# Performance work log

Hardware: AMD Instinct MI355X
Metric: run time of the kernel (lower is better)

Reference implementation:

```python
import jax, jax.numpy as jnp
import numpy as np

B, L, H = 2, 2048, 2048
NH, KVH = 16, 4
D = H // NH          # 128
G = NH // KVH        # 4 query heads per kv head
LN_EPS = 1e-12


def setup_inputs() -> dict:
    key = jax.random.key(0)
    ks = jax.random.split(key, 6)
    s = 0.02
    return {
        "hidden_state": jax.random.normal(ks[0], (B, L, H), jnp.float32),
        "mask": jnp.zeros((B, 1, 1, L), jnp.float32),
        "Wq": jax.random.normal(ks[1], (H, H), jnp.float32) * s,
        "bq": jnp.zeros((H,), jnp.float32),
        "Wk": jax.random.normal(ks[2], (KVH * D, H), jnp.float32) * s,
        "bk": jnp.zeros((KVH * D,), jnp.float32),
        "Wv": jax.random.normal(ks[3], (KVH * D, H), jnp.float32) * s,
        "bv": jnp.zeros((KVH * D,), jnp.float32),
        "Wo": jax.random.normal(ks[4], (H, H), jnp.float32) * s,
        "bo": jnp.zeros((H,), jnp.float32),
        "ln_g": jnp.ones((H,), jnp.float32),
        "ln_b": jnp.zeros((H,), jnp.float32),
    }


def _layernorm(x, g, b):
    mu = jnp.mean(x, axis=-1, keepdims=True)
    var = jnp.mean(jnp.square(x - mu), axis=-1, keepdims=True)
    return (x - mu) * jax.lax.rsqrt(var + LN_EPS) * g + b


def reference(hidden_state, mask, Wq, bq, Wk, bk, Wv, bv, Wo, bo, ln_g, ln_b):
    x = hidden_state
    # projections: b l (h d)
    q = x @ Wq.T + bq            # [B,L,NH*D]
    k = x @ Wk.T + bk            # [B,L,KVH*D]
    v = x @ Wv.T + bv            # [B,L,KVH*D]
    # b l (h d) -> b h l d, with q heads grouped per kv head (GQA broadcast,
    # mathematically identical to repeat_kv + dense SDPA)
    q = q.reshape(B, L, KVH, G, D).transpose(0, 2, 3, 1, 4)   # [B,KVH,G,L,D]
    k = k.reshape(B, L, KVH, D).transpose(0, 2, 1, 3)         # [B,KVH,L,D]
    v = v.reshape(B, L, KVH, D).transpose(0, 2, 1, 3)         # [B,KVH,L,D]
    scale = 1.0 / jnp.sqrt(jnp.float32(D))
    scores = jnp.einsum('bkgld,bkmd->bkglm', q, k) * scale    # [B,KVH,G,L,L]
    scores = scores + mask[:, :, None]                         # broadcast [B,1,1,1,L]
    attn = jax.nn.softmax(scores, axis=-1)
    out = jnp.einsum('bkglm,bkmd->bkgld', attn, v)            # [B,KVH,G,L,D]
    out = out.transpose(0, 3, 1, 2, 4).reshape(B, L, H)       # b h l d -> b l (h d)
    # SelfOutput: dense + residual + layernorm
    out = out @ Wo.T + bo
    return _layernorm(out + x, ln_g, ln_b)
```

## Files before the change

kernel.cpp:

```cpp
#include <hip/hip_runtime.h>
#include <math.h>

typedef short v8s __attribute__((ext_vector_type(8)));
typedef float v4f __attribute__((ext_vector_type(4)));
typedef unsigned long long ull;

constexpr int L_ = 2048;
constexpr int H_ = 2048;
constexpr float LOG2E = 1.4426950408889634f;
constexpr float QSCALE = 0.08838834764831845f * LOG2E;

__device__ inline unsigned short f2bf(float f) {
    unsigned int u = __float_as_uint(f);
    u += 0x7fffu + ((u >> 16) & 1u);
    return (unsigned short)(u >> 16);
}

__device__ inline void async16(const void* g, void* l) {
    __builtin_amdgcn_global_load_lds(
        (const __attribute__((address_space(1))) unsigned int*)g,
        (__attribute__((address_space(3))) unsigned int*)l, 16, 0, 0);
}

__global__ __launch_bounds__(256) void conv_f32_bf16(
    const float* __restrict__ src, unsigned short* __restrict__ dst, int n8)
{
    int i = blockIdx.x * 256 + threadIdx.x;
    if (i >= n8) return;
    float4 a = *(const float4*)(src + (size_t)i * 8);
    float4 b = *(const float4*)(src + (size_t)i * 8 + 4);
    v8s o;
    o[0] = (short)f2bf(a.x); o[1] = (short)f2bf(a.y);
    o[2] = (short)f2bf(a.z); o[3] = (short)f2bf(a.w);
    o[4] = (short)f2bf(b.x); o[5] = (short)f2bf(b.y);
    o[6] = (short)f2bf(b.z); o[7] = (short)f2bf(b.w);
    *(v8s*)(dst + (size_t)i * 8) = o;
}

template <int MODE>
__global__ __launch_bounds__(256) void gemm_mfma(
    const unsigned short* __restrict__ A, const unsigned short* __restrict__ W,
    const float* __restrict__ b0, const float* __restrict__ b1,
    const float* __restrict__ b2,
    unsigned short* __restrict__ oq, unsigned short* __restrict__ ok,
    unsigned short* __restrict__ ovt,
    float* __restrict__ of, const float* __restrict__ resid,
    int K, int N)
{
    __shared__ short A_s[128 * 32];
    __shared__ short B_s[128 * 32];

    const int tid  = threadIdx.x;
    const int lane = tid & 63;
    const int wave = tid >> 6;
    const int lid  = lane & 15;
    const int g    = lane >> 4;
    const int wr   = wave >> 1, wc = wave & 1;
    const int row0 = blockIdx.y * 128, col0 = blockIdx.x * 128;

    v4f acc[4][4];
#pragma unroll
    for (int i = 0; i < 4; ++i)
#pragma unroll
        for (int j = 0; j < 4; ++j) acc[i][j] = (v4f){0.f, 0.f, 0.f, 0.f};

    for (int k0 = 0; k0 < K; k0 += 32) {
        __syncthreads();
#pragma unroll
        for (int i = 0; i < 2; ++i) {
            int idx = tid + i * 256;
            int r = idx >> 2, s = idx & 3;
            int c = s ^ ((r >> 1) & 3);
            async16(A + (size_t)(row0 + r) * K + k0 + c * 8, &A_s[idx * 8]);
            async16(W + (size_t)(col0 + r) * K + k0 + c * 8, &B_s[idx * 8]);
        }
        __syncthreads();

        v8s af[4], bf[4];
#pragma unroll
        for (int t = 0; t < 4; ++t) {
            int ra = wr * 64 + t * 16 + lid;
            int rb = wc * 64 + t * 16 + lid;
            af[t] = *(const v8s*)&A_s[ra * 32 + ((g ^ ((ra >> 1) & 3)) * 8)];
            bf[t] = *(const v8s*)&B_s[rb * 32 + ((g ^ ((rb >> 1) & 3)) * 8)];
        }
#pragma unroll
        for (int mt = 0; mt < 4; ++mt)
#pragma unroll
            for (int nt = 0; nt < 4; ++nt)
                acc[mt][nt] = __builtin_amdgcn_mfma_f32_16x16x32_bf16(
                    af[mt], bf[nt], acc[mt][nt], 0, 0, 0);
    }

    const int crow = row0 + wr * 64, ccol = col0 + wc * 64;
    if (MODE == 0) {
#pragma unroll
        for (int mt = 0; mt < 4; ++mt)
#pragma unroll
            for (int nt = 0; nt < 4; ++nt) {
                int cc = ccol + nt * 16 + lid;
                float bb = b0[cc];
#pragma unroll
                for (int r = 0; r < 4; ++r) {
                    int rr = crow + mt * 16 + g * 4 + r;
                    of[(size_t)rr * N + cc] =
                        acc[mt][nt][r] + bb + resid[(size_t)rr * N + cc];
                }
            }
    } else {
        const int seg = (col0 < 2048) ? 0 : (col0 < 2560 ? 1 : 2);
#pragma unroll
        for (int mt = 0; mt < 4; ++mt)
#pragma unroll
            for (int nt = 0; nt < 4; ++nt) {
                int cc = ccol + nt * 16 + lid;
                if (seg == 0) {
                    float bb = b0[cc];
#pragma unroll
                    for (int r = 0; r < 4; ++r) {
                        int rr = crow + mt * 16 + g * 4 + r;
                        oq[(size_t)rr * 2048 + cc] =
                            f2bf((acc[mt][nt][r] + bb) * QSCALE);
                    }
                } else if (seg == 1) {
                    float bb = b1[cc - 2048];
#pragma unroll
                    for (int r = 0; r < 4; ++r) {
                        int rr = crow + mt * 16 + g * 4 + r;
                        ok[(size_t)rr * 512 + (cc - 2048)] =
                            f2bf(acc[mt][nt][r] + bb);
                    }
                } else {
                    float bb = b2[cc - 2560];
#pragma unroll
                    for (int r = 0; r < 4; ++r) {
                        int rr = crow + mt * 16 + g * 4 + r;
                        ovt[((size_t)((rr >> 11) * 512 + (cc - 2560))) * 2048 +
                            (rr & 2047)] = f2bf(acc[mt][nt][r] + bb);
                    }
                }
            }
    }
}

__global__ __launch_bounds__(256) void flash_mfma(
    const unsigned short* __restrict__ Q,
    const unsigned short* __restrict__ K,
    const unsigned short* __restrict__ Vt,
    const float* __restrict__ mask,
    unsigned short* __restrict__ AO)
{
    __shared__ short K_s[64 * 128];
    __shared__ short V_s[128 * 64];
    __shared__ short P_s[128 * 64];
    __shared__ float mask_s[64];
    __shared__ float alpha_s[128];
    __shared__ float l_s[128];

    const int tid  = threadIdx.x;
    const int lane = tid & 63;
    const int wave = tid >> 6;
    const int lid  = lane & 15;
    const int g    = lane >> 4;
    const int h    = blockIdx.y;
    const int b    = blockIdx.z;
    const int kvh  = h >> 2;
    const int q0   = blockIdx.x * 128;
    const int wq   = wave * 32;

    v8s bq[2][4];
    {
        const size_t base = ((size_t)(b * L_ + q0 + wq + lid)) * 2048 + h * 128;
#pragma unroll
        for (int qt = 0; qt < 2; ++qt)
#pragma unroll
            for (int kc = 0; kc < 4; ++kc)
                bq[qt][kc] = *(const v8s*)(Q + base + (size_t)qt * 16 * 2048 +
                                           kc * 32 + g * 8);
    }

    v4f oacc[2][8];
#pragma unroll
    for (int mt = 0; mt < 2; ++mt)
#pragma unroll
        for (int nt = 0; nt < 8; ++nt) oacc[mt][nt] = (v4f){0.f, 0.f, 0.f, 0.f};
    float m2[2] = {-1e30f, -1e30f};
    float lsm[2] = {0.f, 0.f};

    for (int k0 = 0; k0 < L_; k0 += 64) {
        __syncthreads();
#pragma unroll
        for (int i = 0; i < 4; ++i) {
            int idx = tid + i * 256;
            int kr = idx >> 4, ks = idx & 15;
            int kc = ks ^ (kr & 15);
            async16(K + ((size_t)(b * L_ + k0 + kr)) * 512 + kvh * 128 + kc * 8,
                    &K_s[idx * 8]);
            int vd = idx >> 3, vs = idx & 7;
            int vc = vs ^ (vd & 7);
            async16(Vt + ((size_t)(b * 512 + kvh * 128 + vd)) * 2048 + k0 + vc * 8,
                    &V_s[idx * 8]);
        }
        if (tid < 16) {
            float4 mv = *(const float4*)(mask + (size_t)b * L_ + k0 + tid * 4);
            mask_s[tid * 4 + 0] = mv.x * LOG2E;
            mask_s[tid * 4 + 1] = mv.y * LOG2E;
            mask_s[tid * 4 + 2] = mv.z * LOG2E;
            mask_s[tid * 4 + 3] = mv.w * LOG2E;
        }
        __syncthreads();

        v4f sacc[4][2];
#pragma unroll
        for (int kt = 0; kt < 4; ++kt)
#pragma unroll
            for (int qt = 0; qt < 2; ++qt) sacc[kt][qt] = (v4f){0.f, 0.f, 0.f, 0.f};
#pragma unroll
        for (int kc = 0; kc < 4; ++kc) {
#pragma unroll
            for (int kt = 0; kt < 4; ++kt) {
                v8s ak = *(const v8s*)&K_s[(kt * 16 + lid) * 128 +
                                           (((kc * 4 + g) ^ lid) * 8)];
#pragma unroll
                for (int qt = 0; qt < 2; ++qt)
                    sacc[kt][qt] = __builtin_amdgcn_mfma_f32_16x16x32_bf16(
                        ak, bq[qt][kc], sacc[kt][qt], 0, 0, 0);
            }
        }

        float pmax[2] = {-1e30f, -1e30f};
#pragma unroll
        for (int kt = 0; kt < 4; ++kt) {
            float4 mk = *(const float4*)&mask_s[kt * 16 + g * 4];
#pragma unroll
            for (int qt = 0; qt < 2; ++qt) {
                sacc[kt][qt][0] += mk.x;
                sacc[kt][qt][1] += mk.y;
                sacc[kt][qt][2] += mk.z;
                sacc[kt][qt][3] += mk.w;
#pragma unroll
                for (int r = 0; r < 4; ++r)
                    pmax[qt] = fmaxf(pmax[qt], sacc[kt][qt][r]);
            }
        }
#pragma unroll
        for (int qt = 0; qt < 2; ++qt) {
            pmax[qt] = fmaxf(pmax[qt], __shfl_xor(pmax[qt], 16));
            pmax[qt] = fmaxf(pmax[qt], __shfl_xor(pmax[qt], 32));
        }
        float alpha[2], lad[2];
#pragma unroll
        for (int qt = 0; qt < 2; ++qt) {
            float mnew = fmaxf(m2[qt], pmax[qt]);
            alpha[qt] = __builtin_amdgcn_exp2f(m2[qt] - mnew);
            m2[qt] = mnew;
            lad[qt] = 0.f;
        }
#pragma unroll
        for (int kt = 0; kt < 4; ++kt)
#pragma unroll
            for (int qt = 0; qt < 2; ++qt)
#pragma unroll
                for (int r = 0; r < 4; ++r) {
                    float e = __builtin_amdgcn_exp2f(sacc[kt][qt][r] - m2[qt]);
                    sacc[kt][qt][r] = e;
                    lad[qt] += e;
                }
#pragma unroll
        for (int qt = 0; qt < 2; ++qt) {
            lad[qt] += __shfl_xor(lad[qt], 16);
            lad[qt] += __shfl_xor(lad[qt], 32);
            lsm[qt] = lsm[qt] * alpha[qt] + lad[qt];
        }

#pragma unroll
        for (int qt = 0; qt < 2; ++qt) {
            int qrow = wq + qt * 16 + lid;
#pragma unroll
            for (int kt = 0; kt < 4; ++kt) {
                ull pk = (ull)f2bf(sacc[kt][qt][0]) |
                         ((ull)f2bf(sacc[kt][qt][1]) << 16) |
                         ((ull)f2bf(sacc[kt][qt][2]) << 32) |
                         ((ull)f2bf(sacc[kt][qt][3]) << 48);
                int chunk = kt * 2 + (g >> 1);
                *(ull*)&P_s[qrow * 64 + ((chunk ^ (lid & 7)) * 8) + (g & 1) * 4] = pk;
            }
        }
        if (lane < 16) {
            alpha_s[wq + lid] = alpha[0];
            alpha_s[wq + 16 + lid] = alpha[1];
        }
        __syncthreads();

#pragma unroll
        for (int mt = 0; mt < 2; ++mt) {
            float4 al = *(const float4*)&alpha_s[wq + mt * 16 + g * 4];
            float a4[4] = {al.x, al.y, al.z, al.w};
#pragma unroll
            for (int nt = 0; nt < 8; ++nt)
#pragma unroll
                for (int r = 0; r < 4; ++r) oacc[mt][nt][r] *= a4[r];
        }
#pragma unroll
        for (int kc2 = 0; kc2 < 2; ++kc2) {
            int slot = ((kc2 * 4 + g) ^ (lid & 7)) * 8;
            v8s ap[2];
#pragma unroll
            for (int mt = 0; mt < 2; ++mt)
                ap[mt] = *(const v8s*)&P_s[(wq + mt * 16 + lid) * 64 + slot];
#pragma unroll
            for (int nt = 0; nt < 8; ++nt) {
                v8s bv = *(const v8s*)&V_s[(nt * 16 + lid) * 64 + slot];
#pragma unroll
                for (int mt = 0; mt < 2; ++mt)
                    oacc[mt][nt] = __builtin_amdgcn_mfma_f32_16x16x32_bf16(
                        ap[mt], bv, oacc[mt][nt], 0, 0, 0);
            }
        }
    }

    if (lane < 16) {
        l_s[wq + lid] = lsm[0];
        l_s[wq + 16 + lid] = lsm[1];
    }
    __syncthreads();
#pragma unroll
    for (int mt = 0; mt < 2; ++mt) {
        float4 lv = *(const float4*)&l_s[wq + mt * 16 + g * 4];
        float linv[4] = {1.f / lv.x, 1.f / lv.y, 1.f / lv.z, 1.f / lv.w};
#pragma unroll
        for (int nt = 0; nt < 8; ++nt)
#pragma unroll
            for (int r = 0; r < 4; ++r) {
                size_t orow = (size_t)(b * L_ + q0 + wq + mt * 16 + g * 4 + r);
                AO[orow * 2048 + h * 128 + nt * 16 + lid] =
                    f2bf(oacc[mt][nt][r] * linv[r]);
            }
    }
}

__global__ __launch_bounds__(256) void ln_kernel(
    const float* __restrict__ P, const float* __restrict__ g,
    const float* __restrict__ bta, float* __restrict__ Out)
{
    const int row = blockIdx.x;
    const int tid = threadIdx.x;
    const float* p = P + (size_t)row * H_;

    float vals[8];
    float s = 0.f;
#pragma unroll
    for (int it = 0; it < 2; ++it) {
        int c = tid * 4 + it * 1024;
        float4 a = *(const float4*)&p[c];
        vals[it * 4 + 0] = a.x; vals[it * 4 + 1] = a.y;
        vals[it * 4 + 2] = a.z; vals[it * 4 + 3] = a.w;
        s += a.x + a.y + a.z + a.w;
    }
    __shared__ float red[4];
    float t = s;
#pragma unroll
    for (int off = 32; off > 0; off >>= 1) t += __shfl_xor(t, off);
    if ((tid & 63) == 0) red[tid >> 6] = t;
    __syncthreads();
    float mean = (red[0] + red[1] + red[2] + red[3]) * (1.f / (float)H_);

    float vsum = 0.f;
#pragma unroll
    for (int i = 0; i < 8; ++i) {
        float d = vals[i] - mean;
        vsum += d * d;
    }
    __syncthreads();
    t = vsum;
#pragma unroll
    for (int off = 32; off > 0; off >>= 1) t += __shfl_xor(t, off);
    if ((tid & 63) == 0) red[tid >> 6] = t;
    __syncthreads();
    float var = (red[0] + red[1] + red[2] + red[3]) * (1.f / (float)H_);
    float rs  = 1.f / sqrtf(var + 1e-12f);

#pragma unroll
    for (int it = 0; it < 2; ++it) {
        int c = tid * 4 + it * 1024;
        float4 gv = *(const float4*)&g[c];
        float4 bv = *(const float4*)&bta[c];
        float4 ov;
        ov.x = (vals[it * 4 + 0] - mean) * rs * gv.x + bv.x;
        ov.y = (vals[it * 4 + 1] - mean) * rs * gv.y + bv.y;
        ov.z = (vals[it * 4 + 2] - mean) * rs * gv.z + bv.z;
        ov.w = (vals[it * 4 + 3] - mean) * rs * gv.w + bv.w;
        *(float4*)&Out[(size_t)row * H_ + c] = ov;
    }
}

extern "C" void kernel_launch(void* const* d_in, const int* in_sizes, int n_in,
                              void* d_out, int out_size, void* d_ws, size_t ws_size,
                              hipStream_t stream)
{
    const float* x    = (const float*)d_in[0];
    const float* mask = (const float*)d_in[1];
    const float* Wq   = (const float*)d_in[2];
    const float* bq   = (const float*)d_in[3];
    const float* Wk   = (const float*)d_in[4];
    const float* bk   = (const float*)d_in[5];
    const float* Wv   = (const float*)d_in[6];
    const float* bv   = (const float*)d_in[7];
    const float* Wo   = (const float*)d_in[8];
    const float* bo   = (const float*)d_in[9];
    const float* lng  = (const float*)d_in[10];
    const float* lnb  = (const float*)d_in[11];
    float* out = (float*)d_out;

    char* ws = (char*)d_ws;
    unsigned short* xb   = (unsigned short*)(ws);
    unsigned short* wqkv = (unsigned short*)(ws + 16777216);
    unsigned short* q    = (unsigned short*)(ws + 29360128);
    unsigned short* k    = (unsigned short*)(ws + 46137344);
    unsigned short* vt   = (unsigned short*)(ws + 50331648);
    unsigned short* ao   = (unsigned short*)(ws + 54525952);
    unsigned short* wob  = (unsigned short*)(ws + 71303168);
    float*          pj   = (float*)(ws);

    dim3 blk(256);
    conv_f32_bf16<<<4096, blk, 0, stream>>>(x,  xb,   1048576);
    conv_f32_bf16<<<2048, blk, 0, stream>>>(Wq, wqkv,            524288);
    conv_f32_bf16<<<512,  blk, 0, stream>>>(Wk, wqkv + 2048*2048, 131072);
    conv_f32_bf16<<<512,  blk, 0, stream>>>(Wv, wqkv + 2560*2048, 131072);
    conv_f32_bf16<<<2048, blk, 0, stream>>>(Wo, wob,             524288);

    gemm_mfma<3><<<dim3(24, 32), blk, 0, stream>>>(
        xb, wqkv, bq, bk, bv, q, k, vt, nullptr, nullptr, 2048, 3072);

    flash_mfma<<<dim3(16, 16, 2), blk, 0, stream>>>(q, k, vt, mask, ao);

    gemm_mfma<0><<<dim3(16, 32), blk, 0, stream>>>(
        ao, wob, bo, nullptr, nullptr, nullptr, nullptr, nullptr, pj, x, 2048, 2048);
    ln_kernel<<<4096, blk, 0, stream>>>(pj, lng, lnb, out);
}
```

Baseline: 427.6 us.

## Pipeline GEMM and flash loads, fuse conversions, add V transpose kernel

```diff
diff --git a/kernel.cpp b/kernel.cpp
--- a/kernel.cpp
+++ b/kernel.cpp
@@ -22,19 +22,39 @@
         (__attribute__((address_space(3))) unsigned int*)l, 16, 0, 0);
 }
 
-__global__ __launch_bounds__(256) void conv_f32_bf16(
-    const float* __restrict__ src, unsigned short* __restrict__ dst, int n8)
-{
-    int i = blockIdx.x * 256 + threadIdx.x;
-    if (i >= n8) return;
-    float4 a = *(const float4*)(src + (size_t)i * 8);
-    float4 b = *(const float4*)(src + (size_t)i * 8 + 4);
+__global__ __launch_bounds__(256) void conv_all(
+    const float* __restrict__ x,  const float* __restrict__ wq,
+    const float* __restrict__ wk, const float* __restrict__ wv,
+    const float* __restrict__ wo, const float* __restrict__ mask,
+    unsigned short* __restrict__ xb, unsigned short* __restrict__ wqkvb,
+    unsigned short* __restrict__ wob, float* __restrict__ maskL)
+{
+    int u = blockIdx.x * 256 + threadIdx.x;
+    const float* s;
+    unsigned short* d;
+    if (u < 1048576)      { s = x  + (size_t)u * 8;             d = xb   + (size_t)u * 8; }
+    else if (u < 1572864) { size_t t = (size_t)(u - 1048576) * 8; s = wq + t; d = wqkvb + t; }
+    else if (u < 1703936) { size_t t = (size_t)(u - 1572864) * 8; s = wk + t; d = wqkvb + (size_t)2048 * 2048 + t; }
+    else if (u < 1835008) { size_t t = (size_t)(u - 1703936) * 8; s = wv + t; d = wqkvb + (size_t)2560 * 2048 + t; }
+    else if (u < 2359296) { size_t t = (size_t)(u - 1835008) * 8; s = wo + t; d = wob + t; }
+    else if (u < 2359808) {
+        int m = (u - 2359296) * 8;
+        float4 a = *(const float4*)(mask + m);
+        float4 b = *(const float4*)(mask + m + 4);
+        float4 oa = {a.x * LOG2E, a.y * LOG2E, a.z * LOG2E, a.w * LOG2E};
+        float4 ob = {b.x * LOG2E, b.y * LOG2E, b.z * LOG2E, b.w * LOG2E};
+        *(float4*)(maskL + m) = oa;
+        *(float4*)(maskL + m + 4) = ob;
+        return;
+    } else return;
+    float4 a = *(const float4*)s;
+    float4 b = *(const float4*)(s + 4);
     v8s o;
     o[0] = (short)f2bf(a.x); o[1] = (short)f2bf(a.y);
     o[2] = (short)f2bf(a.z); o[3] = (short)f2bf(a.w);
     o[4] = (short)f2bf(b.x); o[5] = (short)f2bf(b.y);
     o[6] = (short)f2bf(b.z); o[7] = (short)f2bf(b.w);
-    *(v8s*)(dst + (size_t)i * 8) = o;
+    *(v8s*)d = o;
 }
 
 template <int MODE>
@@ -43,12 +63,11 @@
     const float* __restrict__ b0, const float* __restrict__ b1,
     const float* __restrict__ b2,
     unsigned short* __restrict__ oq, unsigned short* __restrict__ ok,
-    unsigned short* __restrict__ ovt,
+    unsigned short* __restrict__ ov,
     float* __restrict__ of, const float* __restrict__ resid,
     int K, int N)
 {
-    __shared__ short A_s[128 * 32];
-    __shared__ short B_s[128 * 32];
+    __shared__ short SM[3 * 8192];
 
     const int tid  = threadIdx.x;
     const int lane = tid & 63;
@@ -58,31 +77,44 @@
     const int wr   = wave >> 1, wc = wave & 1;
     const int row0 = blockIdx.y * 128, col0 = blockIdx.x * 128;
 
-    v4f acc[4][4];
-#pragma unroll
-    for (int i = 0; i < 4; ++i)
-#pragma unroll
-        for (int j = 0; j < 4; ++j) acc[i][j] = (v4f){0.f, 0.f, 0.f, 0.f};
-
-    for (int k0 = 0; k0 < K; k0 += 32) {
-        __syncthreads();
+    auto stage = [&](int k0, int buf) {
 #pragma unroll
         for (int i = 0; i < 2; ++i) {
             int idx = tid + i * 256;
             int r = idx >> 2, s = idx & 3;
             int c = s ^ ((r >> 1) & 3);
-            async16(A + (size_t)(row0 + r) * K + k0 + c * 8, &A_s[idx * 8]);
-            async16(W + (size_t)(col0 + r) * K + k0 + c * 8, &B_s[idx * 8]);
-        }
+            async16(A + (size_t)(row0 + r) * K + k0 + c * 8,
+                    &SM[buf * 8192 + idx * 8]);
+            async16(W + (size_t)(col0 + r) * K + k0 + c * 8,
+                    &SM[buf * 8192 + 4096 + idx * 8]);
+        }
+    };
+
+    v4f acc[4][4];
+#pragma unroll
+    for (int i = 0; i < 4; ++i)
+#pragma unroll
+        for (int j = 0; j < 4; ++j) acc[i][j] = (v4f){0.f, 0.f, 0.f, 0.f};
+
+    stage(0, 0);
+    stage(32, 1);
+    int p = 0;
+    for (int k0 = 0; k0 < K; k0 += 32) {
         __syncthreads();
+        if (k0 + 64 < K) {
+            int nb = p + 2; if (nb >= 3) nb -= 3;
+            stage(k0 + 64, nb);
+        }
+        const short* As = &SM[p * 8192];
+        const short* Bs = &SM[p * 8192 + 4096];
 
         v8s af[4], bf[4];
 #pragma unroll
         for (int t = 0; t < 4; ++t) {
             int ra = wr * 64 + t * 16 + lid;
             int rb = wc * 64 + t * 16 + lid;
-            af[t] = *(const v8s*)&A_s[ra * 32 + ((g ^ ((ra >> 1) & 3)) * 8)];
-            bf[t] = *(const v8s*)&B_s[rb * 32 + ((g ^ ((rb >> 1) & 3)) * 8)];
+            af[t] = *(const v8s*)&As[ra * 32 + ((g ^ ((ra >> 1) & 3)) * 8)];
+            bf[t] = *(const v8s*)&Bs[rb * 32 + ((g ^ ((rb >> 1) & 3)) * 8)];
         }
 #pragma unroll
         for (int mt = 0; mt < 4; ++mt)
@@ -90,6 +122,7 @@
             for (int nt = 0; nt < 4; ++nt)
                 acc[mt][nt] = __builtin_amdgcn_mfma_f32_16x16x32_bf16(
                     af[mt], bf[nt], acc[mt][nt], 0, 0, 0);
+        if (++p == 3) p = 0;
     }
 
     const int crow = row0 + wr * 64, ccol = col0 + wc * 64;
@@ -135,11 +168,36 @@
 #pragma unroll
                     for (int r = 0; r < 4; ++r) {
                         int rr = crow + mt * 16 + g * 4 + r;
-                        ovt[((size_t)((rr >> 11) * 512 + (cc - 2560))) * 2048 +
-                            (rr & 2047)] = f2bf(acc[mt][nt][r] + bb);
+                        ov[(size_t)rr * 512 + (cc - 2560)] =
+                            f2bf(acc[mt][nt][r] + bb);
                     }
                 }
             }
+    }
+}
+
+__global__ __launch_bounds__(256) void transpose_v(
+    const unsigned short* __restrict__ V, unsigned short* __restrict__ Vt)
+{
+    __shared__ unsigned short T[64][72];
+    const int r0 = blockIdx.y * 64;
+    const int c0 = blockIdx.x * 64;
+    const int tid = threadIdx.x;
+    const int r = tid >> 3, c8 = (tid & 7) * 8;
+#pragma unroll
+    for (int h = 0; h < 2; ++h) {
+        v8s val = *(const v8s*)&V[(size_t)(r0 + h * 32 + r) * 512 + c0 + c8];
+#pragma unroll
+        for (int e = 0; e < 8; ++e) T[c8 + e][h * 32 + r] = (unsigned short)val[e];
+    }
+    __syncthreads();
+#pragma unroll
+    for (int h = 0; h < 2; ++h) {
+        int idx = tid + h * 256;
+        int ci = idx >> 3, ch = (idx & 7) * 8;
+        v8s o = *(const v8s*)&T[ci][ch];
+        int rr = r0 + ch;
+        *(v8s*)&Vt[((size_t)((rr >> 11) * 512 + c0 + ci)) * 2048 + (rr & 2047)] = o;
     }
 }
 
@@ -147,13 +205,12 @@
     const unsigned short* __restrict__ Q,
     const unsigned short* __restrict__ K,
     const unsigned short* __restrict__ Vt,
-    const float* __restrict__ mask,
+    const float* __restrict__ maskL,
     unsigned short* __restrict__ AO)
 {
-    __shared__ short K_s[64 * 128];
-    __shared__ short V_s[128 * 64];
-    __shared__ short P_s[128 * 64];
-    __shared__ float mask_s[64];
+    __shared__ short K_s[2][32 * 128];
+    __shared__ short V_s[2][128 * 32];
+    __shared__ short P_s[128 * 32];
     __shared__ float alpha_s[128];
     __shared__ float l_s[128];
 
@@ -168,6 +225,21 @@
     const int q0   = blockIdx.x * 128;
     const int wq   = wave * 32;
 
+    auto stage = [&](int k0, int buf) {
+#pragma unroll
+        for (int i = 0; i < 2; ++i) {
+            int idx = tid + i * 256;
+            int kr = idx >> 4, ks = idx & 15;
+            async16(K + ((size_t)(b * L_ + k0 + kr)) * 512 + kvh * 128 +
+                        ((ks ^ (kr & 15)) * 8),
+                    &K_s[buf][idx * 8]);
+            int vd = idx >> 2, vs = idx & 3;
+            async16(Vt + ((size_t)(b * 512 + kvh * 128 + vd)) * 2048 + k0 +
+                         ((vs ^ (vd & 3)) * 8),
+                    &V_s[buf][idx * 8]);
+        }
+    };
+
     v8s bq[2][4];
     {
         const size_t base = ((size_t)(b * L_ + q0 + wq + lid)) * 2048 + h * 128;
@@ -187,51 +259,34 @@
     float m2[2] = {-1e30f, -1e30f};
     float lsm[2] = {0.f, 0.f};
 
-    for (int k0 = 0; k0 < L_; k0 += 64) {
+    stage(0, 0);
+    for (int it = 0; it < 64; ++it) {
+        const int p = it & 1;
+        const int k0 = it * 32;
         __syncthreads();
-#pragma unroll
-        for (int i = 0; i < 4; ++i) {
-            int idx = tid + i * 256;
-            int kr = idx >> 4, ks = idx & 15;
-            int kc = ks ^ (kr & 15);
-            async16(K + ((size_t)(b * L_ + k0 + kr)) * 512 + kvh * 128 + kc * 8,
-                    &K_s[idx * 8]);
-            int vd = idx >> 3, vs = idx & 7;
-            int vc = vs ^ (vd & 7);
-            async16(Vt + ((size_t)(b * 512 + kvh * 128 + vd)) * 2048 + k0 + vc * 8,
-                    &V_s[idx * 8]);
-        }
-        if (tid < 16) {
-            float4 mv = *(const float4*)(mask + (size_t)b * L_ + k0 + tid * 4);
-            mask_s[tid * 4 + 0] = mv.x * LOG2E;
-            mask_s[tid * 4 + 1] = mv.y * LOG2E;
-            mask_s[tid * 4 + 2] = mv.z * LOG2E;
-            mask_s[tid * 4 + 3] = mv.w * LOG2E;
-        }
-        __syncthreads();
-
-        v4f sacc[4][2];
-#pragma unroll
-        for (int kt = 0; kt < 4; ++kt)
+        if (it + 1 < 64) stage(k0 + 32, p ^ 1);
+
+        v4f sacc[2][2];
+#pragma unroll
+        for (int kt = 0; kt < 2; ++kt)
 #pragma unroll
             for (int qt = 0; qt < 2; ++qt) sacc[kt][qt] = (v4f){0.f, 0.f, 0.f, 0.f};
 #pragma unroll
-        for (int kc = 0; kc < 4; ++kc) {
-#pragma unroll
-            for (int kt = 0; kt < 4; ++kt) {
-                v8s ak = *(const v8s*)&K_s[(kt * 16 + lid) * 128 +
-                                           (((kc * 4 + g) ^ lid) * 8)];
+        for (int kc = 0; kc < 4; ++kc)
+#pragma unroll
+            for (int kt = 0; kt < 2; ++kt) {
+                v8s ak = *(const v8s*)&K_s[p][(kt * 16 + lid) * 128 +
+                                              (((kc * 4 + g) ^ lid) * 8)];
 #pragma unroll
                 for (int qt = 0; qt < 2; ++qt)
                     sacc[kt][qt] = __builtin_amdgcn_mfma_f32_16x16x32_bf16(
                         ak, bq[qt][kc], sacc[kt][qt], 0, 0, 0);
             }
-        }
 
         float pmax[2] = {-1e30f, -1e30f};
 #pragma unroll
-        for (int kt = 0; kt < 4; ++kt) {
-            float4 mk = *(const float4*)&mask_s[kt * 16 + g * 4];
+        for (int kt = 0; kt < 2; ++kt) {
+            float4 mk = *(const float4*)&maskL[b * L_ + k0 + kt * 16 + g * 4];
 #pragma unroll
             for (int qt = 0; qt < 2; ++qt) {
                 sacc[kt][qt][0] += mk.x;
@@ -248,6 +303,7 @@
             pmax[qt] = fmaxf(pmax[qt], __shfl_xor(pmax[qt], 16));
             pmax[qt] = fmaxf(pmax[qt], __shfl_xor(pmax[qt], 32));
         }
+        const ull need = __ballot((pmax[0] > m2[0]) || (pmax[1] > m2[1]));
         float alpha[2], lad[2];
 #pragma unroll
         for (int qt = 0; qt < 2; ++qt) {
@@ -257,7 +313,7 @@
             lad[qt] = 0.f;
         }
 #pragma unroll
-        for (int kt = 0; kt < 4; ++kt)
+        for (int kt = 0; kt < 2; ++kt)
 #pragma unroll
             for (int qt = 0; qt < 2; ++qt)
 #pragma unroll
@@ -277,45 +333,44 @@
         for (int qt = 0; qt < 2; ++qt) {
             int qrow = wq + qt * 16 + lid;
 #pragma unroll
-            for (int kt = 0; kt < 4; ++kt) {
+            for (int kt = 0; kt < 2; ++kt) {
                 ull pk = (ull)f2bf(sacc[kt][qt][0]) |
                          ((ull)f2bf(sacc[kt][qt][1]) << 16) |
                          ((ull)f2bf(sacc[kt][qt][2]) << 32) |
                          ((ull)f2bf(sacc[kt][qt][3]) << 48);
-                int chunk = kt * 2 + (g >> 1);
-                *(ull*)&P_s[qrow * 64 + ((chunk ^ (lid & 7)) * 8) + (g & 1) * 4] = pk;
-            }
-        }
-        if (lane < 16) {
-            alpha_s[wq + lid] = alpha[0];
-            alpha_s[wq + 16 + lid] = alpha[1];
-        }
-        __syncthreads();
-
-#pragma unroll
-        for (int mt = 0; mt < 2; ++mt) {
-            float4 al = *(const float4*)&alpha_s[wq + mt * 16 + g * 4];
-            float a4[4] = {al.x, al.y, al.z, al.w};
-#pragma unroll
-            for (int nt = 0; nt < 8; ++nt)
-#pragma unroll
-                for (int r = 0; r < 4; ++r) oacc[mt][nt][r] *= a4[r];
-        }
-#pragma unroll
-        for (int kc2 = 0; kc2 < 2; ++kc2) {
-            int slot = ((kc2 * 4 + g) ^ (lid & 7)) * 8;
-            v8s ap[2];
+                int slot = (kt * 2 + (g >> 1)) ^ (lid & 3);
+                *(ull*)&P_s[qrow * 32 + slot * 8 + (g & 1) * 4] = pk;
+            }
+        }
+        if (need != 0) {
+            if (lane < 16) {
+                alpha_s[wq + lid] = alpha[0];
+                alpha_s[wq + 16 + lid] = alpha[1];
+            }
+#pragma unroll
+            for (int mt = 0; mt < 2; ++mt) {
+                float4 al = *(const float4*)&alpha_s[wq + mt * 16 + g * 4];
+                float a4[4] = {al.x, al.y, al.z, al.w};
+#pragma unroll
+                for (int nt = 0; nt < 8; ++nt)
+#pragma unroll
+                    for (int r = 0; r < 4; ++r) oacc[mt][nt][r] *= a4[r];
+            }
+        }
+
+        v8s ap[2];
+#pragma unroll
+        for (int mt = 0; mt < 2; ++mt)
+            ap[mt] = *(const v8s*)&P_s[(wq + mt * 16 + lid) * 32 +
+                                       ((g ^ (lid & 3)) * 8)];
+#pragma unroll
+        for (int nt = 0; nt < 8; ++nt) {
+            v8s bv = *(const v8s*)&V_s[p][(nt * 16 + lid) * 32 +
+                                          ((g ^ (lid & 3)) * 8)];
 #pragma unroll
             for (int mt = 0; mt < 2; ++mt)
-                ap[mt] = *(const v8s*)&P_s[(wq + mt * 16 + lid) * 64 + slot];
-#pragma unroll
-            for (int nt = 0; nt < 8; ++nt) {
-                v8s bv = *(const v8s*)&V_s[(nt * 16 + lid) * 64 + slot];
-#pragma unroll
-                for (int mt = 0; mt < 2; ++mt)
-                    oacc[mt][nt] = __builtin_amdgcn_mfma_f32_16x16x32_bf16(
-                        ap[mt], bv, oacc[mt][nt], 0, 0, 0);
-            }
+                oacc[mt][nt] = __builtin_amdgcn_mfma_f32_16x16x32_bf16(
+                    ap[mt], bv, oacc[mt][nt], 0, 0, 0);
         }
     }
 
@@ -413,26 +468,27 @@
     float* out = (float*)d_out;
 
     char* ws = (char*)d_ws;
-    unsigned short* xb   = (unsigned short*)(ws);
-    unsigned short* wqkv = (unsigned short*)(ws + 16777216);
-    unsigned short* q    = (unsigned short*)(ws + 29360128);
-    unsigned short* k    = (unsigned short*)(ws + 46137344);
-    unsigned short* vt   = (unsigned short*)(ws + 50331648);
-    unsigned short* ao   = (unsigned short*)(ws + 54525952);
-    unsigned short* wob  = (unsigned short*)(ws + 71303168);
-    float*          pj   = (float*)(ws);
+    unsigned short* xb    = (unsigned short*)(ws);
+    unsigned short* wqkv  = (unsigned short*)(ws + 16777216);
+    float*          maskL = (float*)         (ws + 29360128);
+    unsigned short* q     = (unsigned short*)(ws + 29376512);
+    unsigned short* k     = (unsigned short*)(ws + 46153728);
+    unsigned short* vnat  = (unsigned short*)(ws + 50348032);
+    unsigned short* vt    = (unsigned short*)(ws + 54542336);
+    unsigned short* ao    = (unsigned short*)(ws + 58736640);
+    unsigned short* wob   = (unsigned short*)(ws + 75513856);
+    float*          pj    = (float*)(ws);
 
     dim3 blk(256);
-    conv_f32_bf16<<<4096, blk, 0, stream>>>(x,  xb,   1048576);
-    conv_f32_bf16<<<2048, blk, 0, stream>>>(Wq, wqkv,            524288);
-    conv_f32_bf16<<<512,  blk, 0, stream>>>(Wk, wqkv + 2048*2048, 131072);
-    conv_f32_bf16<<<512,  blk, 0, stream>>>(Wv, wqkv + 2560*2048, 131072);
-    conv_f32_bf16<<<2048, blk, 0, stream>>>(Wo, wob,             524288);
+    conv_all<<<9218, blk, 0, stream>>>(x, Wq, Wk, Wv, Wo, mask,
+                                       xb, wqkv, wob, maskL);
 
     gemm_mfma<3><<<dim3(24, 32), blk, 0, stream>>>(
-        xb, wqkv, bq, bk, bv, q, k, vt, nullptr, nullptr, 2048, 3072);
-
-    flash_mfma<<<dim3(16, 16, 2), blk, 0, stream>>>(q, k, vt, mask, ao);
+        xb, wqkv, bq, bk, bv, q, k, vnat, nullptr, nullptr, 2048, 3072);
+
+    transpose_v<<<dim3(8, 64), blk, 0, stream>>>(vnat, vt);
+
+    flash_mfma<<<dim3(16, 16, 2), blk, 0, stream>>>(q, k, vt, maskL, ao);
 
     gemm_mfma<0><<<dim3(16, 32), blk, 0, stream>>>(
         ao, wob, bo, nullptr, nullptr, nullptr, nullptr, nullptr, pj, x, 2048, 2048);
```

Measured after the change: 388.1 us. -9.2%, faster.
